# Optimization experiments

Measured on AMD Instinct MI355X. Metric: run time of the kernel, lower is better.

## Reference

```python
import jax, jax.numpy as jnp
import numpy as np

B, N, FIN, E, OUT, NH = 8, 1024, 128, 128, 128, 8
HD = E // NH  # head_dim = 16


def setup_inputs() -> dict:
    key = jax.random.key(0)
    ks = jax.random.split(key, 8)
    s = 0.05
    H = jax.random.normal(ks[0], (B, N, FIN), jnp.float32)
    # binary adjacency (sparse-ish graph), stored dense float as the module expects
    A = (jax.random.uniform(ks[1], (B, N, N)) < 0.05).astype(jnp.float32)
    W_lin = jax.random.normal(ks[2], (FIN, E), jnp.float32) * s
    b_lin = jnp.zeros((E,), jnp.float32)
    # nn.MultiheadAttention packed in-projection (q,k,v) and out-projection
    W_in = jax.random.normal(ks[3], (E, 3 * E), jnp.float32) * s
    b_in = jnp.zeros((3 * E,), jnp.float32)
    W_out = jax.random.normal(ks[4], (E, E), jnp.float32) * s
    b_out = jnp.zeros((E,), jnp.float32)
    W_fin = jax.random.normal(ks[5], (E, OUT), jnp.float32) * s
    b_fin = jnp.zeros((OUT,), jnp.float32)
    return dict(H=H, A=A, W_lin=W_lin, b_lin=b_lin, W_in=W_in, b_in=b_in,
                W_out=W_out, b_out=b_out, W_fin=W_fin, b_fin=b_fin)


def reference(H, A, W_lin, b_lin, W_in, b_in, W_out, b_out, W_fin, b_fin):
    # input projection: Linear(128, embed_dim)
    Hp = H @ W_lin + b_lin                                   # (B,N,E)
    # adjacency-gated attention weights: bmm -> LeakyReLU(0.2) -> *A -> softmax
    s = jnp.einsum('bnd,bmd->bnm', Hp, Hp)                   # (B,N,N)
    s = jnp.where(s >= 0, s, 0.2 * s)
    attn_w = jax.nn.softmax(s * A, axis=-1)                  # (B,N,N)
    # nn.MultiheadAttention self-attention with float attn_mask (ADDED to scores)
    qkv = Hp @ W_in + b_in                                   # (B,N,3E)
    q, k, v = jnp.split(qkv, 3, axis=-1)
    q = q.reshape(B, N, NH, HD)
    k = k.reshape(B, N, NH, HD)
    v = v.reshape(B, N, NH, HD)
    scores = jnp.einsum('bnhd,bmhd->bhnm', q, k) / np.sqrt(HD).astype(np.float32)
    scores = scores + attn_w[:, None]                        # mask broadcast over heads
    p = jax.nn.softmax(scores, axis=-1)                      # (B,NH,N,N)
    o = jnp.einsum('bhnm,bmhd->bnhd', p, v).reshape(B, N, E)
    o = o @ W_out + b_out                                    # MHA out_proj
    # output linear; dropout is identity in eval mode
    return o @ W_fin + b_fin                                 # (B,N,OUT)
```

## Files before the change

### kernel.cpp

```cpp
#include <hip/hip_runtime.h>
#include <hip/hip_bf16.h>


using u16 = unsigned short;
typedef short bf16x8 __attribute__((ext_vector_type(8)));
typedef float f32x4 __attribute__((ext_vector_type(4)));
typedef _Float16 f16;
typedef _Float16 f16x4 __attribute__((ext_vector_type(4)));

#define MFMA16(a, b, c) __builtin_amdgcn_mfma_f32_16x16x16f16(a, b, c, 0, 0, 0)
#define MFMAB(a, b, c) __builtin_amdgcn_mfma_f32_16x16x32_bf16(a, b, c, 0, 0, 0)

__device__ __forceinline__ u16 f2b(float f) {
    unsigned u = __float_as_uint(f);
    return (u16)((u + 0x7fffu + ((u >> 16) & 1u)) >> 16);
}
__device__ __forceinline__ float b2f(u16 u) {
    return __uint_as_float(((unsigned)u) << 16);
}

__global__ void prep_hp(const float* __restrict__ H, const float* __restrict__ Wlin,
                        const float* __restrict__ Win,
                        const float* __restrict__ Wout, const float* __restrict__ Wfin,
                        const float* __restrict__ bout, const float* __restrict__ bfin,
                        const float* __restrict__ blin,
                        u16* __restrict__ WinTb, u16* __restrict__ WcombTb,
                        float* __restrict__ bcomb, float* __restrict__ rowsum,
                        u16* __restrict__ Hpb) {
    if (blockIdx.x < 64) {
        const int m0 = blockIdx.x * 128;
        const int t = threadIdx.x;
        const int wave = t >> 6, lane = t & 63;
        const int wm = (wave >> 1) * 64, wn = (wave & 1) * 64;
        const int m16 = lane & 15, kq = lane >> 4;
        f32x4 acc[4][4] = {};

#pragma unroll
        for (int kc = 0; kc < 4; ++kc) {
            bf16x8 af[4], bf[4];
#pragma unroll
            for (int i = 0; i < 4; ++i) {
                const float* ap = &H[(long long)(m0 + wm + i * 16 + m16) * 128 + kc * 32 + kq * 8];
                float4 u0 = *(const float4*)ap;
                float4 u1 = *(const float4*)(ap + 4);
                bf16x8 a;
                a[0] = (short)f2b(u0.x); a[1] = (short)f2b(u0.y);
                a[2] = (short)f2b(u0.z); a[3] = (short)f2b(u0.w);
                a[4] = (short)f2b(u1.x); a[5] = (short)f2b(u1.y);
                a[6] = (short)f2b(u1.z); a[7] = (short)f2b(u1.w);
                af[i] = a;
            }
#pragma unroll
            for (int j = 0; j < 4; ++j) {
                const int col = wn + j * 16 + m16;
                const int k0 = kc * 32 + kq * 8;
                bf16x8 bb;
#pragma unroll
                for (int e = 0; e < 8; ++e)
                    bb[e] = (short)f2b(Wlin[(long long)(k0 + e) * 128 + col]);
                bf[j] = bb;
            }
#pragma unroll
            for (int i = 0; i < 4; ++i)
#pragma unroll
                for (int j = 0; j < 4; ++j)
                    acc[i][j] = MFMAB(af[i], bf[j], acc[i][j]);
        }
#pragma unroll
        for (int i = 0; i < 4; ++i) {
#pragma unroll
            for (int r = 0; r < 4; ++r) {
                long long row = m0 + wm + i * 16 + kq * 4 + r;
#pragma unroll
                for (int j = 0; j < 4; ++j) {
                    int col = wn + j * 16 + m16;
                    Hpb[row * 128 + col] = f2b(acc[i][j][r] + blin[col]);
                }
            }
        }
        return;
    }
    int i = (blockIdx.x - 64) * 256 + threadIdx.x;
    if (i < 8192) rowsum[i] = 0.f;
    if (i >= 16384 && i < 65536) {
        int k = i - 16384;
        int r = k / 384, c = k - r * 384;
        WinTb[c * 128 + r] = f2b(Win[k]);
    } else if (i >= 65536) {
        int k = i - 65536;
        int o = k & 127, e = k >> 7;
        float s = 0.f;
        for (int kk = 0; kk < 128; ++kk)
            s = fmaf(Wout[e * 128 + kk], Wfin[kk * 128 + o], s);
        WcombTb[o * 128 + e] = f2b(s);
        if (e == 0) {
            float sb = bfin[o];
            for (int kk = 0; kk < 128; ++kk)
                sb = fmaf(bout[kk], Wfin[kk * 128 + o], sb);
            bcomb[o] = sb;
        }
    }
}

__global__ __launch_bounds__(256)
void mfma_qkvz(const u16* __restrict__ Hpb, const u16* __restrict__ WinTb,
               const float* __restrict__ bin, f16* __restrict__ Cq,
               const float* __restrict__ Aadj, u16* __restrict__ EZ,
               float* __restrict__ rowsum) {
    const int blk = blockIdx.x;
    const int t = threadIdx.x;
    const int wave = t >> 6, lane = t & 63;
    const int wm = (wave >> 1) * 64, wn = (wave & 1) * 64;
    const int m16 = lane & 15, kq = lane >> 4;
    f32x4 acc[4][4] = {};

    if (blk < 512) {
        const int b = blk >> 6, mt = (blk >> 3) & 7, nt = blk & 7;
        const u16* Ab = Hpb + (long long)b * 1024 * 128;
        const int m0 = mt * 128, n0 = nt * 128;
#pragma unroll
        for (int kc = 0; kc < 4; ++kc) {
            bf16x8 af[4], bf[4];
#pragma unroll
            for (int i = 0; i < 4; ++i)
                af[i] = *(const bf16x8*)&Ab[(long long)(m0 + wm + i * 16 + m16) * 128 + kc * 32 + kq * 8];
#pragma unroll
            for (int j = 0; j < 4; ++j)
                bf[j] = *(const bf16x8*)&Ab[(long long)(n0 + wn + j * 16 + m16) * 128 + kc * 32 + kq * 8];
#pragma unroll
            for (int i = 0; i < 4; ++i)
#pragma unroll
                for (int j = 0; j < 4; ++j)
                    acc[i][j] = MFMAB(af[i], bf[j], acc[i][j]);
        }
        const long long zb = (long long)b * 1024 * 1024;
#pragma unroll
        for (int i = 0; i < 4; ++i) {
#pragma unroll
            for (int r = 0; r < 4; ++r) {
                int row = m0 + wm + i * 16 + kq * 4 + r;
                float es = 0.f;
#pragma unroll
                for (int j = 0; j < 4; ++j) {
                    int col = n0 + wn + j * 16 + m16;
                    float v = acc[i][j][r];
                    v = v >= 0.f ? v : 0.2f * v;
                    if (Aadj[zb + (long long)row * 1024 + col] == 0.f) v = 0.f;
                    float ev = __expf(v);
                    EZ[zb + (long long)row * 1024 + col] = f2b(ev);
                    es += ev;
                }
#pragma unroll
                for (int off = 1; off < 16; off <<= 1) es += __shfl_xor(es, off);
                if (m16 == 0) atomicAdd(&rowsum[b * 1024 + row], es);
            }
        }
    } else {
        const int q = blk - 512;
        const int mt = q & 63, slab = q >> 6;
        const int m0 = mt * 128;
        const u16* Bslab = WinTb + (long long)slab * 128 * 128;
#pragma unroll
        for (int kc = 0; kc < 4; ++kc) {
            bf16x8 af[4], bf[4];
#pragma unroll
            for (int i = 0; i < 4; ++i)
                af[i] = *(const bf16x8*)&Hpb[(long long)(m0 + wm + i * 16 + m16) * 128 + kc * 32 + kq * 8];
#pragma unroll
            for (int j = 0; j < 4; ++j)
                bf[j] = *(const bf16x8*)&Bslab[(long long)(wn + j * 16 + m16) * 128 + kc * 32 + kq * 8];
#pragma unroll
            for (int i = 0; i < 4; ++i)
#pragma unroll
                for (int j = 0; j < 4; ++j)
                    acc[i][j] = MFMAB(af[i], bf[j], acc[i][j]);
        }
        const float qscale = (slab == 0) ? 0.25f : 1.f;
#pragma unroll
        for (int i = 0; i < 4; ++i) {
#pragma unroll
            for (int r = 0; r < 4; ++r) {
                long long row = m0 + wm + i * 16 + kq * 4 + r;
#pragma unroll
                for (int j = 0; j < 4; ++j) {
                    int col = wn + j * 16 + m16;
                    float v = (acc[i][j][r] + bin[slab * 128 + col]) * qscale;
                    Cq[row * 384 + slab * 128 + col] = (f16)v;
                }
            }
        }
    }
}

__global__ __launch_bounds__(256)
void flash_mfma(const f16* __restrict__ qkv, const u16* __restrict__ ez,
                const float* __restrict__ rowsum, u16* __restrict__ ob) {
    const int n0 = blockIdx.x * 64;
    const int b = blockIdx.y;
    const int h0 = blockIdx.z * 2;
    const int t = threadIdx.x;
    const int w = t >> 6, lane = t & 63;
    const int qr16 = lane & 15, quad = lane >> 4;

    __shared__ u16 Ks[64 * 40];
    __shared__ u16 VTs[32 * 76];
    __shared__ u16 AWs[64 * 72];

    const int qrow_l = w * 16 + qr16;
    const long long qrow_g = b * 1024 + n0 + qrow_l;
    const float inv0 = 1.f / rowsum[qrow_g];

    f16x4 qf[2];
#pragma unroll
    for (int hh = 0; hh < 2; ++hh)
        qf[hh] = *(const f16x4*)&qkv[qrow_g * 384 + (h0 + hh) * 16 + quad * 4];

    f32x4 accO[2] = {};
    float lacc[2] = {0.f, 0.f};

    for (int st = 0; st < 16; ++st) {
        const int kb = st * 64;
        __syncthreads();
        {
            const int key = t >> 2, c8 = t & 3;
            *(uint4*)&Ks[key * 40 + c8 * 8] =
                *(const uint4*)&qkv[((long long)(b * 1024 + kb + key)) * 384 + 128 + h0 * 16 + c8 * 8];
            const f16* vsrc = &qkv[((long long)(b * 1024 + kb + key)) * 384 + 256 + h0 * 16 + c8 * 8];
            f16x4 v0 = *(const f16x4*)vsrc;
            f16x4 v1 = *(const f16x4*)(vsrc + 4);
            const int d0 = c8 * 8;
#pragma unroll
            for (int i = 0; i < 4; ++i) {
                VTs[(d0 + i) * 76 + key] = ((const u16*)&v0)[i];
                VTs[(d0 + 4 + i) * 76 + key] = ((const u16*)&v1)[i];
            }
        }
#pragma unroll
        for (int rr = 0; rr < 2; ++rr) {
            int idx = rr * 256 + t;
            int row = idx >> 3, c16 = idx & 7;
            *(uint4*)&AWs[row * 72 + c16 * 8] =
                *(const uint4*)&ez[((long long)(b * 1024 + n0 + row)) * 1024 + kb + c16 * 8];
        }
        __syncthreads();

#pragma unroll 2
        for (int kt = 0; kt < 4; ++kt) {
            ushort4 ue = *(const ushort4*)&AWs[qrow_l * 72 + kt * 16 + quad * 4];
            f32x4 aw0;
            aw0[0] = b2f(ue.x) * inv0; aw0[1] = b2f(ue.y) * inv0;
            aw0[2] = b2f(ue.z) * inv0; aw0[3] = b2f(ue.w) * inv0;
#pragma unroll
            for (int hh = 0; hh < 2; ++hh) {
                f16x4 kf = *(const f16x4*)&Ks[(kt * 16 + qr16) * 40 + hh * 16 + quad * 4];
                f32x4 s4 = MFMA16(kf, qf[hh], aw0);
                float p0 = __expf(s4[0]), p1 = __expf(s4[1]);
                float p2 = __expf(s4[2]), p3 = __expf(s4[3]);
                lacc[hh] += (p0 + p1) + (p2 + p3);
                f16x4 pf;
                pf[0] = (f16)p0; pf[1] = (f16)p1; pf[2] = (f16)p2; pf[3] = (f16)p3;
                f16x4 vf = *(const f16x4*)&VTs[(hh * 16 + qr16) * 76 + kt * 16 + quad * 4];
                accO[hh] = MFMA16(vf, pf, accO[hh]);
            }
        }
    }
#pragma unroll
    for (int hh = 0; hh < 2; ++hh) {
        float l = lacc[hh];
        l += __shfl_xor(l, 16);
        l += __shfl_xor(l, 32);
        float inv = 1.f / l;
        ushort4 st4;
        st4.x = f2b(accO[hh][0] * inv);
        st4.y = f2b(accO[hh][1] * inv);
        st4.z = f2b(accO[hh][2] * inv);
        st4.w = f2b(accO[hh][3] * inv);
        *(ushort4*)&ob[qrow_g * 128 + (h0 + hh) * 16 + quad * 4] = st4;
    }
}

__global__ __launch_bounds__(256)
void mfma_out(const u16* __restrict__ A, const u16* __restrict__ Bb,
              const float* __restrict__ bias, float* __restrict__ C) {
    const int m0 = blockIdx.x * 128;
    const int t = threadIdx.x;
    const int wave = t >> 6, lane = t & 63;
    const int wm = (wave >> 1) * 64, wn = (wave & 1) * 64;
    const int m16 = lane & 15, kq = lane >> 4;
    f32x4 acc[4][4] = {};

#pragma unroll
    for (int kc = 0; kc < 4; ++kc) {
        bf16x8 af[4], bf[4];
#pragma unroll
        for (int i = 0; i < 4; ++i)
            af[i] = *(const bf16x8*)&A[(long long)(m0 + wm + i * 16 + m16) * 128 + kc * 32 + kq * 8];
#pragma unroll
        for (int j = 0; j < 4; ++j)
            bf[j] = *(const bf16x8*)&Bb[(long long)(wn + j * 16 + m16) * 128 + kc * 32 + kq * 8];
#pragma unroll
        for (int i = 0; i < 4; ++i)
#pragma unroll
            for (int j = 0; j < 4; ++j)
                acc[i][j] = MFMAB(af[i], bf[j], acc[i][j]);
    }
#pragma unroll
    for (int i = 0; i < 4; ++i) {
#pragma unroll
        for (int r = 0; r < 4; ++r) {
            long long row = m0 + wm + i * 16 + kq * 4 + r;
#pragma unroll
            for (int j = 0; j < 4; ++j) {
                int col = wn + j * 16 + m16;
                C[row * 128 + col] = acc[i][j][r] + bias[col];
            }
        }
    }
}

extern "C" void kernel_launch(void* const* d_in, const int* in_sizes, int n_in,
                              void* d_out, int out_size, void* d_ws, size_t ws_size,
                              hipStream_t stream) {
    (void)in_sizes; (void)n_in; (void)out_size; (void)ws_size;
    const float* H    = (const float*)d_in[0];
    const float* Aadj = (const float*)d_in[1];
    const float* Wlin = (const float*)d_in[2];
    const float* blin = (const float*)d_in[3];
    const float* Win  = (const float*)d_in[4];
    const float* bin  = (const float*)d_in[5];
    const float* Wout = (const float*)d_in[6];
    const float* bout = (const float*)d_in[7];
    const float* Wfin = (const float*)d_in[8];
    const float* bfin = (const float*)d_in[9];
    float* out = (float*)d_out;
    char* ws = (char*)d_ws;

    u16*   WinTb   = (u16*)(ws + 0);
    u16*   WcombTb = (u16*)(ws + 98304);
    float* bcomb   = (float*)(ws + 131072);
    float* rowsum  = (float*)(ws + 131584);
    u16*   Hpb     = (u16*)(ws + 262144);
    f16*   qkv     = (f16*)(ws + 2359296);
    u16*   ob      = (u16*)(ws + 8650752);
    u16*   ez      = (u16*)(ws + 12845056);

    prep_hp<<<384, 256, 0, stream>>>(H, Wlin, Win, Wout, Wfin, bout, bfin,
                                     blin, WinTb, WcombTb, bcomb, rowsum, Hpb);
    mfma_qkvz<<<704, 256, 0, stream>>>(Hpb, WinTb, bin, qkv, Aadj, ez, rowsum);
    flash_mfma<<<dim3(16, 8, 4), 256, 0, stream>>>(qkv, ez, rowsum, ob);
    mfma_out<<<64, 256, 0, stream>>>(ob, WcombTb, bcomb, out);
}
```

Baseline: 159.8 us.

## Double-buffer flash attention tiles with register prefetch and larger key blocks

The flash attention kernel now processes 128 keys per stage instead of 64 and keeps two LDS buffers. Global loads for the next K/V/adjacency tile are issued into registers before the current tile is computed, so memory latency can overlap the MFMA work. The stage loop also needs only one barrier instead of two. The cost is more LDS per block (about 60KB), which may reduce occupancy, plus extra register pressure from the prefetch buffers.

Result: slower. 190.6 us (+19.3%).

```diff
diff --git a/kernel.cpp b/kernel.cpp
--- a/kernel.cpp
+++ b/kernel.cpp
@@ -202,9 +202,9 @@
     const int w = t >> 6, lane = t & 63;
     const int qr16 = lane & 15, quad = lane >> 4;
 
-    __shared__ u16 Ks[64 * 40];
-    __shared__ u16 VTs[32 * 76];
-    __shared__ u16 AWs[64 * 72];
+    __shared__ u16 Ks[2][128 * 40];
+    __shared__ u16 VTs[2][32 * 134];
+    __shared__ u16 AWs[2][64 * 136];
 
     const int qrow_l = w * 16 + qr16;
     const long long qrow_g = b * 1024 + n0 + qrow_l;
@@ -218,48 +218,58 @@
     f32x4 accO[2] = {};
     float lacc[2] = {0.f, 0.f};
 
-    for (int st = 0; st < 16; ++st) {
-        const int kb = st * 64;
+    const int key0 = t >> 2, c8 = t & 3;
+    const int awr = t >> 4, awc = t & 15;
+
+    uint4 kreg[2], vreg[2], awreg[4];
+#define FLASH_ISSUE(ST)                                                              \
+    {                                                                                \
+        const int kb_ = (ST) * 128;                                                  \
+        _Pragma("unroll")                                                            \
+        for (int kk = 0; kk < 2; ++kk) {                                             \
+            const long long kr = (long long)(b * 1024 + kb_ + key0 + kk * 64) * 384; \
+            kreg[kk] = *(const uint4*)&qkv[kr + 128 + h0 * 16 + c8 * 8];             \
+            vreg[kk] = *(const uint4*)&qkv[kr + 256 + h0 * 16 + c8 * 8];             \
+        }                                                                            \
+        _Pragma("unroll")                                                            \
+        for (int rr = 0; rr < 4; ++rr)                                               \
+            awreg[rr] = *(const uint4*)&ez[((long long)(b * 1024 + n0 + awr + rr * 16)) * 1024 + kb_ + awc * 8]; \
+    }
+
+    FLASH_ISSUE(0)
+    for (int st = 0; st < 8; ++st) {
+        const int bu = st & 1;
+#pragma unroll
+        for (int kk = 0; kk < 2; ++kk) {
+            *(uint4*)&Ks[bu][(key0 + kk * 64) * 40 + c8 * 8] = kreg[kk];
+            const u16* vp = (const u16*)&vreg[kk];
+            const int d0 = c8 * 8, key = key0 + kk * 64;
+#pragma unroll
+            for (int i = 0; i < 8; ++i)
+                VTs[bu][(d0 + i) * 134 + key] = vp[i];
+        }
+#pragma unroll
+        for (int rr = 0; rr < 4; ++rr)
+            *(uint4*)&AWs[bu][(awr + rr * 16) * 136 + awc * 8] = awreg[rr];
+        if (st < 7) FLASH_ISSUE(st + 1)
         __syncthreads();
-        {
-            const int key = t >> 2, c8 = t & 3;
-            *(uint4*)&Ks[key * 40 + c8 * 8] =
-                *(const uint4*)&qkv[((long long)(b * 1024 + kb + key)) * 384 + 128 + h0 * 16 + c8 * 8];
-            const f16* vsrc = &qkv[((long long)(b * 1024 + kb + key)) * 384 + 256 + h0 * 16 + c8 * 8];
-            f16x4 v0 = *(const f16x4*)vsrc;
-            f16x4 v1 = *(const f16x4*)(vsrc + 4);
-            const int d0 = c8 * 8;
-#pragma unroll
-            for (int i = 0; i < 4; ++i) {
-                VTs[(d0 + i) * 76 + key] = ((const u16*)&v0)[i];
-                VTs[(d0 + 4 + i) * 76 + key] = ((const u16*)&v1)[i];
-            }
-        }
-#pragma unroll
-        for (int rr = 0; rr < 2; ++rr) {
-            int idx = rr * 256 + t;
-            int row = idx >> 3, c16 = idx & 7;
-            *(uint4*)&AWs[row * 72 + c16 * 8] =
-                *(const uint4*)&ez[((long long)(b * 1024 + n0 + row)) * 1024 + kb + c16 * 8];
-        }
-        __syncthreads();
 
 #pragma unroll 2
-        for (int kt = 0; kt < 4; ++kt) {
-            ushort4 ue = *(const ushort4*)&AWs[qrow_l * 72 + kt * 16 + quad * 4];
+        for (int kt = 0; kt < 8; ++kt) {
+            ushort4 ue = *(const ushort4*)&AWs[bu][qrow_l * 136 + kt * 16 + quad * 4];
             f32x4 aw0;
             aw0[0] = b2f(ue.x) * inv0; aw0[1] = b2f(ue.y) * inv0;
             aw0[2] = b2f(ue.z) * inv0; aw0[3] = b2f(ue.w) * inv0;
 #pragma unroll
             for (int hh = 0; hh < 2; ++hh) {
-                f16x4 kf = *(const f16x4*)&Ks[(kt * 16 + qr16) * 40 + hh * 16 + quad * 4];
+                f16x4 kf = *(const f16x4*)&Ks[bu][(kt * 16 + qr16) * 40 + hh * 16 + quad * 4];
                 f32x4 s4 = MFMA16(kf, qf[hh], aw0);
                 float p0 = __expf(s4[0]), p1 = __expf(s4[1]);
                 float p2 = __expf(s4[2]), p3 = __expf(s4[3]);
                 lacc[hh] += (p0 + p1) + (p2 + p3);
                 f16x4 pf;
                 pf[0] = (f16)p0; pf[1] = (f16)p1; pf[2] = (f16)p2; pf[3] = (f16)p3;
-                f16x4 vf = *(const f16x4*)&VTs[(hh * 16 + qr16) * 76 + kt * 16 + quad * 4];
+                f16x4 vf = *(const f16x4*)&VTs[bu][(hh * 16 + qr16) * 134 + kt * 16 + quad * 4];
                 accO[hh] = MFMA16(vf, pf, accO[hh]);
             }
         }
@@ -277,6 +287,7 @@
         st4.w = f2b(accO[hh][3] * inv);
         *(ushort4*)&ob[qrow_g * 128 + (h0 + hh) * 16 + quad * 4] = st4;
     }
+#undef FLASH_ISSUE
 }
 
 __global__ __launch_bounds__(256)
```
